# Performance work log

Measured on AMD Instinct MI355X. Metric: run time of the kernel, lower is better.

## Reference

```python
import jax, jax.numpy as jnp
import numpy as np

EPS = 1e-6

def _phi(x):
    # elu_feature_map: elu(x) + 1 (strictly positive kernel features)
    return jax.nn.elu(x) + 1.0

def setup_inputs() -> dict:
    key = jax.random.key(0)
    kq, kk, kv = jax.random.split(key, 3)
    shape = (8, 2048, 16, 64)  # [batch, seq, heads, head_dim]
    return {
        "q": jax.random.normal(kq, shape, dtype=jnp.float32),
        "k": jax.random.normal(kk, shape, dtype=jnp.float32),
        "v": jax.random.normal(kv, shape, dtype=jnp.float32),
    }

def _causal_linear_attention(q, k, v):
    # q,k,v: [n,l,h,d]. Causal linear attention via cumulative kv-state recurrence.
    # Normalizer z_t = q_t . (sum_{s<=t} k_s)
    z = jnp.einsum('nlhd,nlhd->nlh', q, jnp.cumsum(k, axis=1)) + EPS
    # Scan over time with carry S_t = sum_{s<=t} k_s v_s^T  -> [n,h,d,m]
    qT = jnp.swapaxes(q, 0, 1)  # [l,n,h,d]
    kT = jnp.swapaxes(k, 0, 1)
    vT = jnp.swapaxes(v, 0, 1)
    n, l, h, d = q.shape
    m = v.shape[-1]
    S0 = jnp.zeros((n, h, d, m), dtype=q.dtype)

    def step(S, qkv_t):
        qt, kt, vt = qkv_t  # [n,h,d], [n,h,d], [n,h,m]
        S = S + jnp.einsum('nhd,nhm->nhdm', kt, vt)
        out_t = jnp.einsum('nhd,nhdm->nhm', qt, S)
        return S, out_t

    _, outs = jax.lax.scan(step, S0, (qT, kT, vT))  # outs: [l,n,h,m]
    out = jnp.swapaxes(outs, 0, 1)  # [n,l,h,m]
    return out / z[..., None]

def reference(q, k, v):
    q = _phi(q)
    k = _phi(k)
    return _causal_linear_attention(q, k, v)
```

## Files before the change

### kernel.cpp

```cpp
#include <hip/hip_runtime.h>
#include <math.h>

#define NBATCH 8
#define SEQL   2048
#define NHEAD  16
#define DDIM   64
#define CHK    128
#define NCHUNK (SEQL / CHK)
#define MH     32
#define NTHREADS 1024
#define EPSV   1e-6f
#define QSTR   72
#define PSTR   132
#define KTSTR  66
#define VSTR   132

typedef float f32x4  __attribute__((ext_vector_type(4)));
typedef short bf16x8 __attribute__((ext_vector_type(8)));

#define MFMA16(a,b,c) __builtin_amdgcn_mfma_f32_16x16x32_bf16((a),(b),(c),0,0,0)

__device__ __forceinline__ float phi(float x) { return x > 0.0f ? x + 1.0f : __expf(x); }

__device__ __forceinline__ unsigned int cvt_pk(float lo, float hi) {
    unsigned int r;
    asm("v_cvt_pk_bf16_f32 %0, %1, %2" : "=v"(r) : "v"(lo), "v"(hi));
    return r;
}
__device__ __forceinline__ ushort f2bf(float x) {
    union { float f; unsigned int i; } t; t.f = x;
    unsigned int r = t.i + 0x7fffu + ((t.i >> 16) & 1u);
    return (ushort)(r >> 16);
}

__device__ __forceinline__ bf16x8 ld16B(const ushort* p) {
    return *reinterpret_cast<const bf16x8*>(p);
}
__device__ __forceinline__ bf16x8 ld8B(const ushort* p) {
    union { bf16x8 v; uint2 u[2]; } x;
    x.u[0] = *(const uint2*)p;
    x.u[1] = *(const uint2*)(p + 4);
    return x.v;
}
__device__ __forceinline__ bf16x8 ld4B(const ushort* p) {
    union { bf16x8 v; unsigned int u[4]; } x;
    const unsigned int* q = (const unsigned int*)p;
    x.u[0] = q[0]; x.u[1] = q[1]; x.u[2] = q[2]; x.u[3] = q[3];
    return x.v;
}

__global__ __launch_bounds__(NTHREADS)
void linattn_mfma3(const float* __restrict__ qg, const float* __restrict__ kg,
                   const float* __restrict__ vg, float* __restrict__ og) {
    __shared__ __align__(16) ushort sQ[CHK][QSTR];
    __shared__ __align__(16) ushort sK[CHK][QSTR];
    __shared__ __align__(16) ushort sP[CHK][PSTR];
    __shared__ __align__(16) ushort sKt[2][2][DDIM][KTSTR];
    __shared__ __align__(16) ushort sVt[2][MH][VSTR];
    __shared__ __align__(16) ushort sStA[MH][QSTR];
    __shared__ __align__(16) ushort sStB[MH][QSTR];
    __shared__ float sKsW[2][16][64];
    __shared__ float sKS[64];
    __shared__ __align__(16) ushort sKSbf[64];

    const int tid = threadIdx.x;
    const int w   = tid >> 6;
    const int l   = tid & 63;
    const int lr  = l & 15;
    const int lk  = l >> 4;
    const int R   = w >> 1;
    const int M2  = w & 1;
    const int t8  = w & 7;
    const int D4  = t8 >> 1;
    const int SM2 = t8 & 1;
    const int kh  = w >> 3;

    const int bid   = blockIdx.x;
    const int nh    = bid & 127;
    const int mhalf = bid >> 7;
    const int n  = nh >> 4;
    const int hh = nh & 15;

    const size_t tstride = (size_t)NHEAD * DDIM;
    const size_t base0 = ((size_t)n * SEQL * NHEAD + hh) * DDIM;
    const float* qb = qg + base0;
    const float* kb = kg + base0;
    const float* vb = vg + base0 + (size_t)mhalf * MH;
    float*       ob = og + base0 + (size_t)mhalf * MH;

    const int qk_row = tid >> 4;
    const int qk_c4  = (tid & 15) << 2;
    const int v_row  = tid >> 3;
    const int v_c4   = (tid & 7) << 2;

    float4 qr[2], kr[2], vr;
    #pragma unroll
    for (int i = 0; i < 2; ++i) {
        qr[i] = *(const float4*)(qb + (size_t)(qk_row + 64 * i) * tstride + qk_c4);
        kr[i] = *(const float4*)(kb + (size_t)(qk_row + 64 * i) * tstride + qk_c4);
    }
    vr = *(const float4*)(vb + (size_t)v_row * tstride + v_c4);

    for (int i = tid; i < CHK * PSTR / 2; i += NTHREADS)
        ((unsigned int*)&sP[0][0])[i] = 0u;
    if (tid < 64) sKS[tid] = 0.0f;

    const f32x4 zero4 = {0.0f, 0.0f, 0.0f, 0.0f};
    f32x4 accS = zero4;
    bf16x8 ones;
    #pragma unroll
    for (int j = 0; j < 8; ++j) ones[j] = (short)0x3F80;

    const int rowb = 16 * R + 4 * lk;

    for (int tc = 0; tc < NCHUNK; ++tc) {
        const int t0 = tc * CHK;
        const int cur = tc & 1, prv = cur ^ 1;

        if (tid < 64) {
            float s = sKS[tid];
            if (tc > 0) {
                #pragma unroll
                for (int ww = 0; ww < 16; ++ww) s += sKsW[prv][ww][tid];
                sKS[tid] = s;
            }
            sKSbf[tid] = f2bf(s);
        }
        float kpart[4] = {0.0f, 0.0f, 0.0f, 0.0f};
        #pragma unroll
        for (int i = 0; i < 2; ++i) {
            const int row = qk_row + 64 * i;
            const float4 q4 = qr[i], k4 = kr[i];
            const float kx = phi(k4.x), ky = phi(k4.y), kz = phi(k4.z), kw = phi(k4.w);
            kpart[0] += kx; kpart[1] += ky; kpart[2] += kz; kpart[3] += kw;
            uint2 qp, kp;
            qp.x = cvt_pk(phi(q4.x), phi(q4.y));
            qp.y = cvt_pk(phi(q4.z), phi(q4.w));
            kp.x = cvt_pk(kx, ky);
            kp.y = cvt_pk(kz, kw);
            *(uint2*)&sQ[row][qk_c4] = qp;
            *(uint2*)&sK[row][qk_c4] = kp;
            ushort* kt = &sKt[cur][i][0][0];
            const int sp = row & 63;
            kt[(qk_c4 + 0) * KTSTR + sp] = (ushort)kp.x;
            kt[(qk_c4 + 1) * KTSTR + sp] = (ushort)(kp.x >> 16);
            kt[(qk_c4 + 2) * KTSTR + sp] = (ushort)kp.y;
            kt[(qk_c4 + 3) * KTSTR + sp] = (ushort)(kp.y >> 16);
        }
        #pragma unroll
        for (int j = 0; j < 4; ++j) {
            kpart[j] += __shfl_xor(kpart[j], 16);
            kpart[j] += __shfl_xor(kpart[j], 32);
        }
        if (l < 16) *(float4*)&sKsW[cur][w][4 * l] = *(float4*)kpart;
        {
            const unsigned int p0 = cvt_pk(vr.x, vr.y), p1 = cvt_pk(vr.z, vr.w);
            sVt[cur][v_c4 + 0][v_row] = (ushort)p0;
            sVt[cur][v_c4 + 1][v_row] = (ushort)(p0 >> 16);
            sVt[cur][v_c4 + 2][v_row] = (ushort)p1;
            sVt[cur][v_c4 + 3][v_row] = (ushort)(p1 >> 16);
        }
        {
            ushort* st = (kh == 0) ? &sStA[0][0] : &sStB[0][0];
            uint2 s2;
            s2.x = cvt_pk(accS[0], accS[1]);
            s2.y = cvt_pk(accS[2], accS[3]);
            *(uint2*)(st + (16 * SM2 + lr) * QSTR + 16 * D4 + 4 * lk) = s2;
        }
        __syncthreads();

        if (tc + 1 < NCHUNK) {
            const int t1 = t0 + CHK;
            #pragma unroll
            for (int i = 0; i < 2; ++i) {
                qr[i] = *(const float4*)(qb + (size_t)(t1 + qk_row + 64 * i) * tstride + qk_c4);
                kr[i] = *(const float4*)(kb + (size_t)(t1 + qk_row + 64 * i) * tstride + qk_c4);
            }
            vr = *(const float4*)(vb + (size_t)(t1 + v_row) * tstride + v_c4);
        }

        const ushort* qrow = &sQ[16 * R + lr][0];
        const bf16x8 aQ0 = ld16B(qrow + 8 * lk);
        const bf16x8 aQ1 = ld16B(qrow + 32 + 8 * lk);

        f32x4 accZ = zero4;
        accZ = MFMA16(aQ0, ld16B(&sKSbf[8 * lk]), accZ);
        accZ = MFMA16(aQ1, ld16B(&sKSbf[32 + 8 * lk]), accZ);

        f32x4 accO = zero4;
        {
            const ushort* sa = &sStA[16 * M2 + lr][0];
            const ushort* sb = &sStB[16 * M2 + lr][0];
            accO = MFMA16(aQ0, ld16B(sa + 8 * lk), accO);
            accO = MFMA16(aQ1, ld16B(sa + 32 + 8 * lk), accO);
            accO = MFMA16(aQ0, ld16B(sb + 8 * lk), accO);
            accO = MFMA16(aQ1, ld16B(sb + 32 + 8 * lk), accO);
        }

        #pragma unroll
        for (int ci = 0; ci < 4; ++ci) {
            const int C4 = 4 * M2 + ci;
            if (C4 > R) continue;
            const ushort* krow = &sK[16 * C4 + lr][0];
            f32x4 acc = zero4;
            acc = MFMA16(aQ0, ld16B(krow + 8 * lk), acc);
            acc = MFMA16(aQ1, ld16B(krow + 32 + 8 * lk), acc);
            if (C4 == R) {
                #pragma unroll
                for (int r = 0; r < 4; ++r)
                    acc[r] = (lr <= 4 * lk + r) ? acc[r] : 0.0f;
            }
            const unsigned int p01 = cvt_pk(acc[0], acc[1]);
            const unsigned int p23 = cvt_pk(acc[2], acc[3]);
            const int col = 16 * C4 + lr;
            sP[rowb + 0][col] = (ushort)p01;
            sP[rowb + 1][col] = (ushort)(p01 >> 16);
            sP[rowb + 2][col] = (ushort)p23;
            sP[rowb + 3][col] = (ushort)(p23 >> 16);
        }
        __syncthreads();

        const ushort* prow = &sP[16 * R + lr][0];
        const ushort* vrow = &sVt[cur][16 * M2 + lr][0];
        #pragma unroll
        for (int ks = 0; ks < 4; ++ks) {
            const bf16x8 aP = ld8B(prow + 32 * ks + 8 * lk);
            accO = MFMA16(aP, ld8B(vrow + 32 * ks + 8 * lk), accO);
            accZ = MFMA16(aP, ones, accZ);
        }
        {
            const ushort* ktr = &sKt[cur][kh][16 * D4 + lr][0];
            const ushort* vsr = &sVt[cur][16 * SM2 + lr][64 * kh];
            #pragma unroll
            for (int ks2 = 0; ks2 < 2; ++ks2) {
                const bf16x8 aK  = ld4B(ktr + 32 * ks2 + 8 * lk);
                const bf16x8 bVs = ld8B(vsr + 32 * ks2 + 8 * lk);
                accS = MFMA16(aK, bVs, accS);
            }
        }
        #pragma unroll
        for (int r = 0; r < 4; ++r) {
            const float zin = __builtin_amdgcn_rcpf(accZ[r] + EPSV);
            ob[(size_t)(t0 + rowb + r) * tstride + 16 * M2 + lr] = accO[r] * zin;
        }
    }
}

extern "C" void kernel_launch(void* const* d_in, const int* in_sizes, int n_in,
                              void* d_out, int out_size, void* d_ws, size_t ws_size,
                              hipStream_t stream) {
    const float* q = (const float*)d_in[0];
    const float* k = (const float*)d_in[1];
    const float* v = (const float*)d_in[2];
    float* o = (float*)d_out;
    dim3 grid(NBATCH * NHEAD * 2);
    linattn_mfma3<<<grid, NTHREADS, 0, stream>>>(q, k, v, o);
}
```

Measured before the change: 62.88 us.

## Switch to 32x32 MFMA with warp-specialized diagonal, off-diagonal and state roles

```diff
diff --git a/kernel.cpp b/kernel.cpp
--- a/kernel.cpp
+++ b/kernel.cpp
@@ -11,14 +11,14 @@
 #define NTHREADS 1024
 #define EPSV   1e-6f
 #define QSTR   72
-#define PSTR   132
-#define KTSTR  66
-#define VSTR   132
-
-typedef float f32x4  __attribute__((ext_vector_type(4)));
-typedef short bf16x8 __attribute__((ext_vector_type(8)));
-
-#define MFMA16(a,b,c) __builtin_amdgcn_mfma_f32_16x16x32_bf16((a),(b),(c),0,0,0)
+#define TSTR   132
+#define SSTR   68
+
+typedef float  f32x16 __attribute__((ext_vector_type(16)));
+typedef float  f32x4v __attribute__((ext_vector_type(4)));
+typedef short  bf16x8 __attribute__((ext_vector_type(8)));
+
+#define MFMA32(a,b,c) __builtin_amdgcn_mfma_f32_32x32x16_bf16((a),(b),(c),0,0,0)
 
 __device__ __forceinline__ float phi(float x) { return x > 0.0f ? x + 1.0f : __expf(x); }
 
@@ -32,33 +32,47 @@
     unsigned int r = t.i + 0x7fffu + ((t.i >> 16) & 1u);
     return (ushort)(r >> 16);
 }
-
-__device__ __forceinline__ bf16x8 ld16B(const ushort* p) {
-    return *reinterpret_cast<const bf16x8*>(p);
-}
+__device__ __forceinline__ float bf2f(short u) {
+    union { unsigned int i; float f; } t;
+    t.i = ((unsigned int)(unsigned short)u) << 16;
+    return t.f;
+}
+__device__ __forceinline__ bf16x8 ld16B(const ushort* p) { return *reinterpret_cast<const bf16x8*>(p); }
 __device__ __forceinline__ bf16x8 ld8B(const ushort* p) {
     union { bf16x8 v; uint2 u[2]; } x;
     x.u[0] = *(const uint2*)p;
     x.u[1] = *(const uint2*)(p + 4);
     return x.v;
 }
-__device__ __forceinline__ bf16x8 ld4B(const ushort* p) {
+__device__ __forceinline__ void pl32swap(unsigned int &a, unsigned int &b) {
+    asm volatile("v_permlane32_swap_b32 %0, %1" : "+v"(a), "+v"(b));
+}
+__device__ __forceinline__ float halfswap_add(float x) {
+    unsigned int a = __float_as_uint(x), b = a;
+    pl32swap(a, b);
+    return __uint_as_float(a) + __uint_as_float(b);
+}
+__device__ __forceinline__ bf16x8 make_pa(float p0,float p1,float p2,float p3,
+                                          float p4,float p5,float p6,float p7) {
+    unsigned int a0 = cvt_pk(p0,p1), b0 = cvt_pk(p4,p5);
+    unsigned int a1 = cvt_pk(p2,p3), b1 = cvt_pk(p6,p7);
+    pl32swap(a0,b0); pl32swap(a1,b1);
     union { bf16x8 v; unsigned int u[4]; } x;
-    const unsigned int* q = (const unsigned int*)p;
-    x.u[0] = q[0]; x.u[1] = q[1]; x.u[2] = q[2]; x.u[3] = q[3];
+    x.u[0]=a0; x.u[1]=a1; x.u[2]=b0; x.u[3]=b1;
     return x.v;
 }
 
 __global__ __launch_bounds__(NTHREADS)
-void linattn_mfma3(const float* __restrict__ qg, const float* __restrict__ kg,
+void linattn_mfma4(const float* __restrict__ qg, const float* __restrict__ kg,
                    const float* __restrict__ vg, float* __restrict__ og) {
     __shared__ __align__(16) ushort sQ[CHK][QSTR];
     __shared__ __align__(16) ushort sK[CHK][QSTR];
-    __shared__ __align__(16) ushort sP[CHK][PSTR];
-    __shared__ __align__(16) ushort sKt[2][2][DDIM][KTSTR];
-    __shared__ __align__(16) ushort sVt[2][MH][VSTR];
-    __shared__ __align__(16) ushort sStA[MH][QSTR];
-    __shared__ __align__(16) ushort sStB[MH][QSTR];
+    __shared__ __align__(16) ushort sKt[DDIM][TSTR];
+    __shared__ __align__(16) ushort sVt[MH][TSTR];
+    __shared__ __align__(16) ushort sSt[2][MH][SSTR];
+    __shared__ __align__(16) float  sOp[6][8][CHK];
+    __shared__ float sZp[6][32];
+    __shared__ float sZt[CHK];
     __shared__ float sKsW[2][16][64];
     __shared__ float sKS[64];
     __shared__ __align__(16) ushort sKSbf[64];
@@ -66,14 +80,8 @@
     const int tid = threadIdx.x;
     const int w   = tid >> 6;
     const int l   = tid & 63;
-    const int lr  = l & 15;
-    const int lk  = l >> 4;
-    const int R   = w >> 1;
-    const int M2  = w & 1;
-    const int t8  = w & 7;
-    const int D4  = t8 >> 1;
-    const int SM2 = t8 & 1;
-    const int kh  = w >> 3;
+    const int l31 = l & 31;
+    const int hi  = l >> 5;
 
     const int bid   = blockIdx.x;
     const int nh    = bid & 127;
@@ -81,167 +89,233 @@
     const int n  = nh >> 4;
     const int hh = nh & 15;
 
-    const size_t tstride = (size_t)NHEAD * DDIM;
     const size_t base0 = ((size_t)n * SEQL * NHEAD + hh) * DDIM;
     const float* qb = qg + base0;
     const float* kb = kg + base0;
     const float* vb = vg + base0 + (size_t)mhalf * MH;
     float*       ob = og + base0 + (size_t)mhalf * MH;
 
-    const int qk_row = tid >> 4;
-    const int qk_c4  = (tid & 15) << 2;
-    const int v_row  = tid >> 3;
-    const int v_c4   = (tid & 7) << 2;
-
-    float4 qr[2], kr[2], vr;
+    const int pidx = w - 4;
+    const int pc = (pidx < 1) ? 1 : (pidx < 3) ? 2 : 3;
+    const int pg = pidx - ((pc == 1) ? 0 : (pc == 2) ? 1 : 3);
+    const int dt = (w - 10) >> 1;
+    const int kh = (w - 10) & 1;
+
+    const int r2 = tid >> 4;
+    const int x4 = (tid & 15) << 2;
+    const int tv  = tid - 512;
+    const int sp2 = (tv >> 3) << 1;
+    const int vm4 = (tv & 7) << 2;
+
+    float4 qrA, qrB, krA, krB, vrA, vrB;
+    qrA = *(const float4*)(qb + (size_t)(2*r2    ) * 1024 + x4);
+    qrB = *(const float4*)(qb + (size_t)(2*r2 + 1) * 1024 + x4);
+    krA = *(const float4*)(kb + (size_t)(2*r2    ) * 1024 + x4);
+    krB = *(const float4*)(kb + (size_t)(2*r2 + 1) * 1024 + x4);
+    if (w >= 8) {
+        vrA = *(const float4*)(vb + (size_t)(sp2    ) * 1024 + vm4);
+        vrB = *(const float4*)(vb + (size_t)(sp2 + 1) * 1024 + vm4);
+    }
+
+    if (w == 14) sKS[l] = 0.0f;
+
+    f32x16 accS;
     #pragma unroll
-    for (int i = 0; i < 2; ++i) {
-        qr[i] = *(const float4*)(qb + (size_t)(qk_row + 64 * i) * tstride + qk_c4);
-        kr[i] = *(const float4*)(kb + (size_t)(qk_row + 64 * i) * tstride + qk_c4);
-    }
-    vr = *(const float4*)(vb + (size_t)v_row * tstride + v_c4);
-
-    for (int i = tid; i < CHK * PSTR / 2; i += NTHREADS)
-        ((unsigned int*)&sP[0][0])[i] = 0u;
-    if (tid < 64) sKS[tid] = 0.0f;
-
-    const f32x4 zero4 = {0.0f, 0.0f, 0.0f, 0.0f};
-    f32x4 accS = zero4;
-    bf16x8 ones;
-    #pragma unroll
-    for (int j = 0; j < 8; ++j) ones[j] = (short)0x3F80;
-
-    const int rowb = 16 * R + 4 * lk;
+    for (int i = 0; i < 16; ++i) accS[i] = 0.0f;
 
     for (int tc = 0; tc < NCHUNK; ++tc) {
         const int t0 = tc * CHK;
         const int cur = tc & 1, prv = cur ^ 1;
 
-        if (tid < 64) {
-            float s = sKS[tid];
+        if (w == 14) {
+            float s = sKS[l];
             if (tc > 0) {
                 #pragma unroll
-                for (int ww = 0; ww < 16; ++ww) s += sKsW[prv][ww][tid];
-                sKS[tid] = s;
-            }
-            sKSbf[tid] = f2bf(s);
-        }
-        float kpart[4] = {0.0f, 0.0f, 0.0f, 0.0f};
-        #pragma unroll
-        for (int i = 0; i < 2; ++i) {
-            const int row = qk_row + 64 * i;
-            const float4 q4 = qr[i], k4 = kr[i];
-            const float kx = phi(k4.x), ky = phi(k4.y), kz = phi(k4.z), kw = phi(k4.w);
-            kpart[0] += kx; kpart[1] += ky; kpart[2] += kz; kpart[3] += kw;
-            uint2 qp, kp;
-            qp.x = cvt_pk(phi(q4.x), phi(q4.y));
-            qp.y = cvt_pk(phi(q4.z), phi(q4.w));
-            kp.x = cvt_pk(kx, ky);
-            kp.y = cvt_pk(kz, kw);
-            *(uint2*)&sQ[row][qk_c4] = qp;
-            *(uint2*)&sK[row][qk_c4] = kp;
-            ushort* kt = &sKt[cur][i][0][0];
-            const int sp = row & 63;
-            kt[(qk_c4 + 0) * KTSTR + sp] = (ushort)kp.x;
-            kt[(qk_c4 + 1) * KTSTR + sp] = (ushort)(kp.x >> 16);
-            kt[(qk_c4 + 2) * KTSTR + sp] = (ushort)kp.y;
-            kt[(qk_c4 + 3) * KTSTR + sp] = (ushort)(kp.y >> 16);
-        }
-        #pragma unroll
-        for (int j = 0; j < 4; ++j) {
-            kpart[j] += __shfl_xor(kpart[j], 16);
-            kpart[j] += __shfl_xor(kpart[j], 32);
-        }
-        if (l < 16) *(float4*)&sKsW[cur][w][4 * l] = *(float4*)kpart;
+                for (int ww = 0; ww < 16; ++ww) s += sKsW[prv][ww][l];
+                sKS[l] = s;
+            }
+            sKSbf[l] = f2bf(s);
+        }
         {
-            const unsigned int p0 = cvt_pk(vr.x, vr.y), p1 = cvt_pk(vr.z, vr.w);
-            sVt[cur][v_c4 + 0][v_row] = (ushort)p0;
-            sVt[cur][v_c4 + 1][v_row] = (ushort)(p0 >> 16);
-            sVt[cur][v_c4 + 2][v_row] = (ushort)p1;
-            sVt[cur][v_c4 + 3][v_row] = (ushort)(p1 >> 16);
-        }
-        {
-            ushort* st = (kh == 0) ? &sStA[0][0] : &sStB[0][0];
-            uint2 s2;
-            s2.x = cvt_pk(accS[0], accS[1]);
-            s2.y = cvt_pk(accS[2], accS[3]);
-            *(uint2*)(st + (16 * SM2 + lr) * QSTR + 16 * D4 + 4 * lk) = s2;
+            const float q0x=phi(qrA.x), q0y=phi(qrA.y), q0z=phi(qrA.z), q0w=phi(qrA.w);
+            const float q1x=phi(qrB.x), q1y=phi(qrB.y), q1z=phi(qrB.z), q1w=phi(qrB.w);
+            uint2 u;
+            u.x = cvt_pk(q0x,q0y); u.y = cvt_pk(q0z,q0w);
+            *(uint2*)&sQ[2*r2][x4] = u;
+            u.x = cvt_pk(q1x,q1y); u.y = cvt_pk(q1z,q1w);
+            *(uint2*)&sQ[2*r2+1][x4] = u;
+
+            const float k0x=phi(krA.x), k0y=phi(krA.y), k0z=phi(krA.z), k0w=phi(krA.w);
+            const float k1x=phi(krB.x), k1y=phi(krB.y), k1z=phi(krB.z), k1w=phi(krB.w);
+            u.x = cvt_pk(k0x,k0y); u.y = cvt_pk(k0z,k0w);
+            *(uint2*)&sK[2*r2][x4] = u;
+            u.x = cvt_pk(k1x,k1y); u.y = cvt_pk(k1z,k1w);
+            *(uint2*)&sK[2*r2+1][x4] = u;
+
+            *(unsigned int*)&sKt[x4+0][2*r2] = cvt_pk(k0x, k1x);
+            *(unsigned int*)&sKt[x4+1][2*r2] = cvt_pk(k0y, k1y);
+            *(unsigned int*)&sKt[x4+2][2*r2] = cvt_pk(k0z, k1z);
+            *(unsigned int*)&sKt[x4+3][2*r2] = cvt_pk(k0w, k1w);
+
+            float kp0 = k0x + k1x, kp1 = k0y + k1y, kp2 = k0z + k1z, kp3 = k0w + k1w;
+            kp0 += __shfl_xor(kp0, 16); kp0 += __shfl_xor(kp0, 32);
+            kp1 += __shfl_xor(kp1, 16); kp1 += __shfl_xor(kp1, 32);
+            kp2 += __shfl_xor(kp2, 16); kp2 += __shfl_xor(kp2, 32);
+            kp3 += __shfl_xor(kp3, 16); kp3 += __shfl_xor(kp3, 32);
+            if (l < 16) {
+                float4 kp = {kp0, kp1, kp2, kp3};
+                *(float4*)&sKsW[cur][w][4*l] = kp;
+            }
+        }
+        if (w >= 8) {
+            *(unsigned int*)&sVt[vm4+0][sp2] = cvt_pk(vrA.x, vrB.x);
+            *(unsigned int*)&sVt[vm4+1][sp2] = cvt_pk(vrA.y, vrB.y);
+            *(unsigned int*)&sVt[vm4+2][sp2] = cvt_pk(vrA.z, vrB.z);
+            *(unsigned int*)&sVt[vm4+3][sp2] = cvt_pk(vrA.w, vrB.w);
+        }
+        if (w >= 10 && w < 14) {
+            ushort* st = &sSt[kh][l31][32*dt];
+            #pragma unroll
+            for (int rg = 0; rg < 4; ++rg) {
+                uint2 s2;
+                s2.x = cvt_pk(accS[4*rg+0], accS[4*rg+1]);
+                s2.y = cvt_pk(accS[4*rg+2], accS[4*rg+3]);
+                *(uint2*)(st + 8*rg + 4*hi) = s2;
+            }
         }
         __syncthreads();
 
         if (tc + 1 < NCHUNK) {
             const int t1 = t0 + CHK;
-            #pragma unroll
-            for (int i = 0; i < 2; ++i) {
-                qr[i] = *(const float4*)(qb + (size_t)(t1 + qk_row + 64 * i) * tstride + qk_c4);
-                kr[i] = *(const float4*)(kb + (size_t)(t1 + qk_row + 64 * i) * tstride + qk_c4);
-            }
-            vr = *(const float4*)(vb + (size_t)(t1 + v_row) * tstride + v_c4);
-        }
-
-        const ushort* qrow = &sQ[16 * R + lr][0];
-        const bf16x8 aQ0 = ld16B(qrow + 8 * lk);
-        const bf16x8 aQ1 = ld16B(qrow + 32 + 8 * lk);
-
-        f32x4 accZ = zero4;
-        accZ = MFMA16(aQ0, ld16B(&sKSbf[8 * lk]), accZ);
-        accZ = MFMA16(aQ1, ld16B(&sKSbf[32 + 8 * lk]), accZ);
-
-        f32x4 accO = zero4;
-        {
-            const ushort* sa = &sStA[16 * M2 + lr][0];
-            const ushort* sb = &sStB[16 * M2 + lr][0];
-            accO = MFMA16(aQ0, ld16B(sa + 8 * lk), accO);
-            accO = MFMA16(aQ1, ld16B(sa + 32 + 8 * lk), accO);
-            accO = MFMA16(aQ0, ld16B(sb + 8 * lk), accO);
-            accO = MFMA16(aQ1, ld16B(sb + 32 + 8 * lk), accO);
-        }
-
-        #pragma unroll
-        for (int ci = 0; ci < 4; ++ci) {
-            const int C4 = 4 * M2 + ci;
-            if (C4 > R) continue;
-            const ushort* krow = &sK[16 * C4 + lr][0];
-            f32x4 acc = zero4;
-            acc = MFMA16(aQ0, ld16B(krow + 8 * lk), acc);
-            acc = MFMA16(aQ1, ld16B(krow + 32 + 8 * lk), acc);
-            if (C4 == R) {
+            qrA = *(const float4*)(qb + (size_t)(t1 + 2*r2    ) * 1024 + x4);
+            qrB = *(const float4*)(qb + (size_t)(t1 + 2*r2 + 1) * 1024 + x4);
+            krA = *(const float4*)(kb + (size_t)(t1 + 2*r2    ) * 1024 + x4);
+            krB = *(const float4*)(kb + (size_t)(t1 + 2*r2 + 1) * 1024 + x4);
+            if (w >= 8) {
+                vrA = *(const float4*)(vb + (size_t)(t1 + sp2    ) * 1024 + vm4);
+                vrB = *(const float4*)(vb + (size_t)(t1 + sp2 + 1) * 1024 + vm4);
+            }
+        }
+
+        f32x16 accO;
+        float zl = 0.0f;
+
+        if (w < 4) {
+            const int c = w;
+            const bf16x8 aQ0 = ld16B(&sQ[32*c + l31][ 0 + 8*hi]);
+            const bf16x8 aQ1 = ld16B(&sQ[32*c + l31][16 + 8*hi]);
+            const bf16x8 aQ2 = ld16B(&sQ[32*c + l31][32 + 8*hi]);
+            const bf16x8 aQ3 = ld16B(&sQ[32*c + l31][48 + 8*hi]);
+
+            f32x16 accP;
+            #pragma unroll
+            for (int i = 0; i < 16; ++i) accP[i] = 0.0f;
+            accP = MFMA32(ld16B(&sK[32*c + l31][ 0 + 8*hi]), aQ0, accP);
+            accP = MFMA32(ld16B(&sK[32*c + l31][16 + 8*hi]), aQ1, accP);
+            accP = MFMA32(ld16B(&sK[32*c + l31][32 + 8*hi]), aQ2, accP);
+            accP = MFMA32(ld16B(&sK[32*c + l31][48 + 8*hi]), aQ3, accP);
+            float rs = 0.0f;
+            #pragma unroll
+            for (int r = 0; r < 16; ++r) {
+                const int srow = (r & 3) + 8 * (r >> 2) + 4 * hi;
+                const float pv = (srow <= l31) ? accP[r] : 0.0f;
+                accP[r] = pv;
+                rs += pv;
+            }
+            const bf16x8 pa0 = make_pa(accP[0],accP[1],accP[2],accP[3],
+                                       accP[4],accP[5],accP[6],accP[7]);
+            const bf16x8 pa1 = make_pa(accP[8],accP[9],accP[10],accP[11],
+                                       accP[12],accP[13],accP[14],accP[15]);
+            #pragma unroll
+            for (int i = 0; i < 16; ++i) accO[i] = 0.0f;
+            accO = MFMA32(pa0, ld8B(&sVt[l31][32*c +  0 + 8*hi]), accO);
+            accO = MFMA32(pa1, ld8B(&sVt[l31][32*c + 16 + 8*hi]), accO);
+            #pragma unroll
+            for (int buf = 0; buf < 2; ++buf) {
+                accO = MFMA32(aQ0, ld8B(&sSt[buf][l31][ 0 + 8*hi]), accO);
+                accO = MFMA32(aQ1, ld8B(&sSt[buf][l31][16 + 8*hi]), accO);
+                accO = MFMA32(aQ2, ld8B(&sSt[buf][l31][32 + 8*hi]), accO);
+                accO = MFMA32(aQ3, ld8B(&sSt[buf][l31][48 + 8*hi]), accO);
+            }
+            float qz = 0.0f;
+            {
+                const bf16x8 ks0 = ld16B(&sKSbf[ 0 + 8*hi]);
+                const bf16x8 ks1 = ld16B(&sKSbf[16 + 8*hi]);
+                const bf16x8 ks2 = ld16B(&sKSbf[32 + 8*hi]);
+                const bf16x8 ks3 = ld16B(&sKSbf[48 + 8*hi]);
                 #pragma unroll
-                for (int r = 0; r < 4; ++r)
-                    acc[r] = (lr <= 4 * lk + r) ? acc[r] : 0.0f;
-            }
-            const unsigned int p01 = cvt_pk(acc[0], acc[1]);
-            const unsigned int p23 = cvt_pk(acc[2], acc[3]);
-            const int col = 16 * C4 + lr;
-            sP[rowb + 0][col] = (ushort)p01;
-            sP[rowb + 1][col] = (ushort)(p01 >> 16);
-            sP[rowb + 2][col] = (ushort)p23;
-            sP[rowb + 3][col] = (ushort)(p23 >> 16);
+                for (int j = 0; j < 8; ++j) {
+                    qz += bf2f(aQ0[j]) * bf2f(ks0[j]);
+                    qz += bf2f(aQ1[j]) * bf2f(ks1[j]);
+                    qz += bf2f(aQ2[j]) * bf2f(ks2[j]);
+                    qz += bf2f(aQ3[j]) * bf2f(ks3[j]);
+                }
+            }
+            zl = halfswap_add(rs + qz);
+        } else if (w < 10) {
+            f32x16 accP;
+            #pragma unroll
+            for (int i = 0; i < 16; ++i) accP[i] = 0.0f;
+            #pragma unroll
+            for (int kk = 0; kk < 4; ++kk)
+                accP = MFMA32(ld16B(&sK[32*pg + l31][16*kk + 8*hi]),
+                              ld16B(&sQ[32*pc + l31][16*kk + 8*hi]), accP);
+            float rs = 0.0f;
+            #pragma unroll
+            for (int r = 0; r < 16; ++r) rs += accP[r];
+            const float zp = halfswap_add(rs);
+            if (hi == 0) sZp[pidx][l31] = zp;
+            const bf16x8 pa0 = make_pa(accP[0],accP[1],accP[2],accP[3],
+                                       accP[4],accP[5],accP[6],accP[7]);
+            const bf16x8 pa1 = make_pa(accP[8],accP[9],accP[10],accP[11],
+                                       accP[12],accP[13],accP[14],accP[15]);
+            f32x16 po;
+            #pragma unroll
+            for (int i = 0; i < 16; ++i) po[i] = 0.0f;
+            po = MFMA32(pa0, ld8B(&sVt[l31][32*pg +  0 + 8*hi]), po);
+            po = MFMA32(pa1, ld8B(&sVt[l31][32*pg + 16 + 8*hi]), po);
+            #pragma unroll
+            for (int rp = 0; rp < 8; ++rp) {
+                float2 t; t.x = po[2*rp]; t.y = po[2*rp+1];
+                *(float2*)&sOp[pidx][rp][2*l] = t;
+            }
+        } else if (w < 14) {
+            #pragma unroll
+            for (int kk = 0; kk < 4; ++kk) {
+                const bf16x8 aK = ld8B(&sKt[32*dt + l31][64*kh + 16*kk + 8*hi]);
+                const bf16x8 bV = ld8B(&sVt[l31][64*kh + 16*kk + 8*hi]);
+                accS = MFMA32(aK, bV, accS);
+            }
         }
         __syncthreads();
 
-        const ushort* prow = &sP[16 * R + lr][0];
-        const ushort* vrow = &sVt[cur][16 * M2 + lr][0];
-        #pragma unroll
-        for (int ks = 0; ks < 4; ++ks) {
-            const bf16x8 aP = ld8B(prow + 32 * ks + 8 * lk);
-            accO = MFMA16(aP, ld8B(vrow + 32 * ks + 8 * lk), accO);
-            accZ = MFMA16(aP, ones, accZ);
-        }
-        {
-            const ushort* ktr = &sKt[cur][kh][16 * D4 + lr][0];
-            const ushort* vsr = &sVt[cur][16 * SM2 + lr][64 * kh];
-            #pragma unroll
-            for (int ks2 = 0; ks2 < 2; ++ks2) {
-                const bf16x8 aK  = ld4B(ktr + 32 * ks2 + 8 * lk);
-                const bf16x8 bVs = ld8B(vsr + 32 * ks2 + 8 * lk);
-                accS = MFMA16(aK, bVs, accS);
-            }
-        }
-        #pragma unroll
-        for (int r = 0; r < 4; ++r) {
-            const float zin = __builtin_amdgcn_rcpf(accZ[r] + EPSV);
-            ob[(size_t)(t0 + rowb + r) * tstride + 16 * M2 + lr] = accO[r] * zin;
+        if (w < 4) {
+            const int c = w;
+            const int p0 = (c == 1) ? 0 : (c == 2) ? 1 : 3;
+            for (int i = 0; i < c; ++i) {
+                const int pp = p0 + i;
+                #pragma unroll
+                for (int rp = 0; rp < 8; ++rp) {
+                    const float2 t = *(const float2*)&sOp[pp][rp][2*l];
+                    accO[2*rp]     += t.x;
+                    accO[2*rp + 1] += t.y;
+                }
+                zl += sZp[pp][l31];
+            }
+            zl += EPSV;
+            if (hi == 0) sZt[32*c + l31] = zl;
+            asm volatile("s_waitcnt lgkmcnt(0)" ::: "memory");
+            __builtin_amdgcn_sched_barrier(0);
+            #pragma unroll
+            for (int rg = 0; rg < 4; ++rg) {
+                const f32x4v z4 = *(const f32x4v*)&sZt[32*c + 8*rg + 4*hi];
+                #pragma unroll
+                for (int rr = 0; rr < 4; ++rr) {
+                    const int row = t0 + 32*c + rr + 8*rg + 4*hi;
+                    ob[(size_t)row * 1024 + l31] =
+                        accO[4*rg + rr] * __builtin_amdgcn_rcpf(z4[rr]);
+                }
+            }
         }
     }
 }
@@ -254,5 +328,5 @@
     const float* v = (const float*)d_in[2];
     float* o = (float*)d_out;
     dim3 grid(NBATCH * NHEAD * 2);
-    linattn_mfma3<<<grid, NTHREADS, 0, stream>>>(q, k, v, o);
-}
+    linattn_mfma4<<<grid, NTHREADS, 0, stream>>>(q, k, v, o);
+}
```

New measurement: 130.0 us. +106.7%, slower.
